# Kernel tuning notes

Hardware: AMD Instinct MI355X
Metric: run time of the kernel (lower is better)

## Reference

```python
import jax, jax.numpy as jnp
import numpy as np

EPS = 1e-05
RMS_EPS = 1e-06


def activation_quant(x, num_bits=8):
    # per-token (last-dim) abs-max int8 fake quant, computed in fp32
    qn = -(2 ** (num_bits - 1))
    qp = 2 ** (num_bits - 1) - 1
    xf = x.astype(jnp.float32)
    s = qp / jnp.clip(jnp.max(jnp.abs(xf), axis=-1, keepdims=True), EPS, None)
    return (jnp.clip(jnp.round(xf * s), qn, qp) / s).astype(x.dtype)


def weight_quant(w):
    # full-tensor abs-mean ternary fake quant
    wf = w.astype(jnp.float32)
    s = 1.0 / jnp.clip(jnp.mean(jnp.abs(wf)), EPS, None)
    return (jnp.clip(jnp.round(wf * s), -1.0, 1.0) / s).astype(w.dtype)


def bit_linear(x, w):
    # STE wrappers (identity in forward value, straight-through in grad)
    qx = x + jax.lax.stop_gradient(activation_quant(x) - x)
    qw = w + jax.lax.stop_gradient(weight_quant(w) - w)
    return jnp.einsum('bsh,oh->bso', qx, qw)


def rms_norm(x, weight, eps=RMS_EPS):
    xf = x.astype(jnp.float32)
    var = jnp.mean(xf * xf, axis=-1, keepdims=True)
    return weight * (xf * jax.lax.rsqrt(var + eps)).astype(x.dtype)


def setup_inputs() -> dict:
    key = jax.random.key(0)
    k1, k2, k3, k4 = jax.random.split(key, 4)
    B, S, H, I = 2, 2048, 2048, 8192
    scale = 1.0 / np.sqrt(H)
    return {
        'x': jax.random.normal(k1, (B, S, H), dtype=jnp.float32),
        'w_gate': jax.random.normal(k2, (I, H), dtype=jnp.float32) * scale,
        'w_up': jax.random.normal(k3, (I, H), dtype=jnp.float32) * scale,
        'w_down': jax.random.normal(k4, (H, I), dtype=jnp.float32) * (1.0 / np.sqrt(I)),
        'ln_weight': jnp.ones((I,), dtype=jnp.float32),
    }


def reference(x, w_gate, w_up, w_down, ln_weight):
    h = jax.nn.silu(bit_linear(x, w_gate)) * bit_linear(x, w_up)
    h = rms_norm(h, ln_weight)
    return bit_linear(h, w_down)
```

## Files before the change

### kernel.cpp

```cpp
#include <hip/hip_runtime.h>
#include <stdint.h>

typedef int v4i __attribute__((ext_vector_type(4)));

#define TOKENS 4096
#define HDIM   2048
#define IDIM   8192
#define WN     16777216
#define NBLK   512
#define BANDP  5e-7f

static __device__ __forceinline__ void gload_lds16(const void* g, void* l) {
  __builtin_amdgcn_global_load_lds(
      (const __attribute__((address_space(1))) void*)(unsigned long long)(uintptr_t)g,
      (__attribute__((address_space(3))) void*)(unsigned)(uintptr_t)l,
      16, 0, 0);
}

static __device__ __forceinline__ double wsum64d(double v) {
#pragma unroll
  for (int m = 32; m; m >>= 1) v += __shfl_xor(v, m, 64);
  return v;
}
static __device__ __forceinline__ double wmax64d(double v) {
#pragma unroll
  for (int m = 32; m; m >>= 1) v = fmax(v, __shfl_xor(v, m, 64));
  return v;
}
static __device__ __forceinline__ float wmax64f(float v) {
#pragma unroll
  for (int m = 32; m; m >>= 1) v = fmaxf(v, __shfl_xor(v, m, 64));
  return v;
}

static __device__ __forceinline__ int q8f(float v, float s, float lo, float hi) {
  float p = v * s;
  return (int)fminf(fmaxf(rintf(p), lo), hi);
}
static __device__ __forceinline__ uint32_t packq_f(float4 v, float s) {
  int a = q8f(v.x, s, -128.f, 127.f);
  int b = q8f(v.y, s, -128.f, 127.f);
  int c = q8f(v.z, s, -128.f, 127.f);
  int d = q8f(v.w, s, -128.f, 127.f);
  return (uint32_t)((a & 255) | ((b & 255) << 8) | ((c & 255) << 16) | ((d & 255) << 24));
}

__global__ __launch_bounds__(256) void wsum_leaf(const float* __restrict__ wg,
                                                 const float* __restrict__ wu,
                                                 const float* __restrict__ wd,
                                                 float* __restrict__ part) {
  const float* w = blockIdx.y == 0 ? wg : (blockIdx.y == 1 ? wu : wd);
  int tid = threadIdx.x;
  const float4* w4 = (const float4*)w;
  size_t base4 = ((size_t)blockIdx.x * 256 + tid) * 32;
  float4 p = w4[base4], q = w4[base4 + 1];
  float r0 = fabsf(p.x), r1 = fabsf(p.y), r2 = fabsf(p.z), r3 = fabsf(p.w);
  float r4 = fabsf(q.x), r5 = fabsf(q.y), r6 = fabsf(q.z), r7 = fabsf(q.w);
  for (int i = 2; i < 32; i += 2) {
    float4 a = w4[base4 + i], b = w4[base4 + i + 1];
    r0 += fabsf(a.x); r1 += fabsf(a.y); r2 += fabsf(a.z); r3 += fabsf(a.w);
    r4 += fabsf(b.x); r5 += fabsf(b.y); r6 += fabsf(b.z); r7 += fabsf(b.w);
  }
  float leaf = ((r0 + r1) + (r2 + r3)) + ((r4 + r5) + (r6 + r7));
  __shared__ float A[256], B[256];
  A[tid] = leaf;
  __syncthreads();
  float* src = A; float* dst = B;
  for (int n = 128; n >= 1; n >>= 1) {
    if (tid < n) dst[tid] = src[2 * tid] + src[2 * tid + 1];
    __syncthreads();
    float* t = src; src = dst; dst = t;
  }
  if (tid == 0) part[blockIdx.y * NBLK + blockIdx.x] = src[0];
}

__global__ __launch_bounds__(256) void wsum_final(const float* __restrict__ part,
                                                  float* __restrict__ wsc) {
  int t = blockIdx.x, tid = threadIdx.x;
  __shared__ float A[512], B[256];
  A[tid] = part[t * NBLK + tid];
  A[tid + 256] = part[t * NBLK + tid + 256];
  __syncthreads();
  float* src = A; float* dst = B;
  for (int n = 256; n >= 1; n >>= 1) {
    if (tid < n) dst[tid] = src[2 * tid] + src[2 * tid + 1];
    __syncthreads();
    float* tmp = src; src = dst; dst = tmp;
  }
  if (tid == 0) {
    float mean32 = src[0] / (float)WN;
    float m32 = fmaxf(mean32, 1e-5f);
    float s32 = 1.0f / m32;
    wsc[t] = s32;
    wsc[3 + t] = 1.0f / s32;
  }
}

__global__ __launch_bounds__(256) void wquant_kernel(const float* __restrict__ wg,
                                                     const float* __restrict__ wu,
                                                     const float* __restrict__ wd,
                                                     const float* __restrict__ wsc,
                                                     int8_t* __restrict__ qg,
                                                     int8_t* __restrict__ qu,
                                                     int8_t* __restrict__ qd) {
  int t = blockIdx.y;
  const float* w = t == 0 ? wg : (t == 1 ? wu : wd);
  int8_t* q = t == 0 ? qg : (t == 1 ? qu : qd);
  float s32 = wsc[t];
  const float4* w4 = (const float4*)w;
  uint32_t* q4 = (uint32_t*)q;
  const int n4 = WN / 4;
  for (int i = blockIdx.x * 256 + threadIdx.x; i < n4; i += gridDim.x * 256) {
    float4 v = w4[i];
    float vv[4] = {v.x, v.y, v.z, v.w};
    int o[4];
#pragma unroll
    for (int j = 0; j < 4; ++j) {
      float pf = fabsf(vv[j]) * s32;
      int q2 = 2 * (int)fminf(rintf(pf), 1.0f);
      if (fabsf(pf - 0.5f) < BANDP) q2 = 1;
      o[j] = (vv[j] < 0.0f) ? -q2 : q2;
    }
    q4[i] = (uint32_t)((o[0] & 255) | ((o[1] & 255) << 8) |
                       ((o[2] & 255) << 16) | ((o[3] & 255) << 24));
  }
}

__global__ __launch_bounds__(256) void xquant_kernel(const float* __restrict__ x,
                                                     int8_t* __restrict__ qx,
                                                     double* __restrict__ axd) {
  int row = blockIdx.x, tid = threadIdx.x;
  const float4* xr = (const float4*)(x + (size_t)row * HDIM);
  float4 v0 = xr[tid], v1 = xr[tid + 256];
  float m = fmaxf(fmaxf(fmaxf(fabsf(v0.x), fabsf(v0.y)), fmaxf(fabsf(v0.z), fabsf(v0.w))),
                  fmaxf(fmaxf(fabsf(v1.x), fabsf(v1.y)), fmaxf(fabsf(v1.z), fabsf(v1.w))));
  m = wmax64f(m);
  __shared__ float red[4];
  int wid = tid >> 6, lane = tid & 63;
  if (lane == 0) red[wid] = m;
  __syncthreads();
  float mm = fmaxf(fmaxf(red[0], red[1]), fmaxf(red[2], red[3]));
  float c32 = fmaxf(mm, 1e-5f);
  float s32 = 127.0f / c32;
  if (tid == 0) axd[row] = 1.0 / (double)s32;
  uint32_t* q4 = (uint32_t*)(qx + (size_t)row * HDIM);
  q4[tid] = packq_f(v0, s32);
  q4[tid + 256] = packq_f(v1, s32);
}

__global__ __launch_bounds__(512, 4) void gemm1_kernel(const int8_t* __restrict__ qx,
                                                       const int8_t* __restrict__ qg,
                                                       const int8_t* __restrict__ qu,
                                                       const float* __restrict__ wsc,
                                                       const double* __restrict__ axd,
                                                       float* __restrict__ h) {
  __shared__ char lds[3 * 8192];
  int tid = threadIdx.x, wid = tid >> 6, lane = tid & 63;
  int l15 = lane & 15, lgp = lane >> 4;
  int wr = wid >> 2, wc = wid & 3;
  int flat = blockIdx.y * 64 + blockIdx.x;
  int nf = (flat & 7) * 256 + (flat >> 3);
  int m0 = (nf >> 6) * 128, n0 = (nf & 63) * 128;
  const int8_t* bA = qx + (size_t)m0 * HDIM;
  const int8_t* bG = qg + (size_t)n0 * HDIM;
  const int8_t* bU = qu + (size_t)n0 * HDIM;

  v4i accg[4][2], accu[4][2];
  v4i vzero = {0, 0, 0, 0};
#pragma unroll
  for (int i = 0; i < 4; ++i)
#pragma unroll
    for (int j = 0; j < 2; ++j) { accg[i][j] = vzero; accu[i][j] = vzero; }

  int aoff[4], goff[2], uoff[2];
#pragma unroll
  for (int i = 0; i < 4; ++i)
    aoff[i] = lgp * 2048 + (wr * 64 + i * 16 + l15) * 16;
#pragma unroll
  for (int i = 0; i < 2; ++i) {
    goff[i] = 8192 + lgp * 2048 + (wc * 32 + i * 16 + l15) * 16;
    uoff[i] = goff[i] + 8192;
  }

  int srow = tid & 127, sslab = tid >> 7;
  char* dA = lds + sslab * 2048 + srow * 16;

  for (int kt = 0; kt < HDIM; kt += 64) {
    __syncthreads();
    size_t koff = (size_t)kt + sslab * 16;
    gload_lds16(bA + (size_t)srow * HDIM + koff, dA);
    gload_lds16(bG + (size_t)srow * HDIM + koff, dA + 8192);
    gload_lds16(bU + (size_t)srow * HDIM + koff, dA + 16384);
    __syncthreads();
    v4i a[4], bg[2], bu[2];
#pragma unroll
    for (int i = 0; i < 4; ++i) a[i] = *(const v4i*)(lds + aoff[i]);
#pragma unroll
    for (int i = 0; i < 2; ++i) {
      bg[i] = *(const v4i*)(lds + goff[i]);
      bu[i] = *(const v4i*)(lds + uoff[i]);
    }
#pragma unroll
    for (int mi = 0; mi < 4; ++mi)
#pragma unroll
      for (int ni = 0; ni < 2; ++ni) {
        accg[mi][ni] = __builtin_amdgcn_mfma_i32_16x16x64_i8(a[mi], bg[ni], accg[mi][ni], 0, 0, 0);
        accu[mi][ni] = __builtin_amdgcn_mfma_i32_16x16x64_i8(a[mi], bu[ni], accu[mi][ni], 0, 0, 0);
      }
  }

  double mg = 0.5 * (double)wsc[3 + 0];
  double mu = 0.5 * (double)wsc[3 + 1];
#pragma unroll
  for (int mi = 0; mi < 4; ++mi) {
#pragma unroll
    for (int rg = 0; rg < 4; ++rg) {
      int grow = m0 + wr * 64 + mi * 16 + lgp * 4 + rg;
      double axr = axd[grow];
      double sg = axr * mg, su = axr * mu;
#pragma unroll
      for (int ni = 0; ni < 2; ++ni) {
        int gcol = n0 + wc * 32 + ni * 16 + l15;
        double g = (double)accg[mi][ni][rg] * sg;
        double u = (double)accu[mi][ni][rg] * su;
        double sig = 1.0 / (1.0 + exp(-g));
        h[(size_t)grow * IDIM + gcol] = (float)((g * sig) * u);
      }
    }
  }
}

__global__ __launch_bounds__(256) void hquant_kernel(const float* __restrict__ h,
                                                     const float* __restrict__ lnw,
                                                     double* __restrict__ ahd,
                                                     int8_t* __restrict__ qh) {
  int row = blockIdx.x, tid = threadIdx.x;
  const float4* hr = (const float4*)(h + (size_t)row * IDIM);
  const float4* lw4 = (const float4*)lnw;
  float4 hv[8], wv[8];
  double ssq = 0.0;
#pragma unroll
  for (int i = 0; i < 8; ++i) {
    hv[i] = hr[tid + i * 256];
    wv[i] = lw4[tid + i * 256];
    ssq += (double)hv[i].x * hv[i].x + (double)hv[i].y * hv[i].y +
           (double)hv[i].z * hv[i].z + (double)hv[i].w * hv[i].w;
  }
  ssq = wsum64d(ssq);
  __shared__ double redd[4];
  __shared__ double redm[4];
  int wid = tid >> 6, lane = tid & 63;
  if (lane == 0) redd[wid] = ssq;
  __syncthreads();
  double tot = redd[0] + redd[1] + redd[2] + redd[3];
  double rd = 1.0 / sqrt(tot * (1.0 / (double)IDIM) + 1e-6);
  double mx = 0.0;
#pragma unroll
  for (int i = 0; i < 8; ++i) {
    double y0 = (double)wv[i].x * ((double)hv[i].x * rd);
    double y1 = (double)wv[i].y * ((double)hv[i].y * rd);
    double y2 = (double)wv[i].z * ((double)hv[i].z * rd);
    double y3 = (double)wv[i].w * ((double)hv[i].w * rd);
    mx = fmax(mx, fmax(fmax(fabs(y0), fabs(y1)), fmax(fabs(y2), fabs(y3))));
  }
  mx = wmax64d(mx);
  if (lane == 0) redm[wid] = mx;
  __syncthreads();
  double mm = fmax(fmax(redm[0], redm[1]), fmax(redm[2], redm[3]));
  float c32 = fmaxf((float)mm, 1e-5f);
  float s32 = 127.0f / c32;
  double sd = (double)s32;
  if (tid == 0) ahd[row] = 1.0 / (double)s32;
  uint32_t* q4 = (uint32_t*)(qh + (size_t)row * IDIM);
#pragma unroll
  for (int i = 0; i < 8; ++i) {
    double y0 = (double)wv[i].x * ((double)hv[i].x * rd);
    double y1 = (double)wv[i].y * ((double)hv[i].y * rd);
    double y2 = (double)wv[i].z * ((double)hv[i].z * rd);
    double y3 = (double)wv[i].w * ((double)hv[i].w * rd);
    int a = (int)fmin(fmax(rint(y0 * sd), -128.0), 127.0);
    int b = (int)fmin(fmax(rint(y1 * sd), -128.0), 127.0);
    int c = (int)fmin(fmax(rint(y2 * sd), -128.0), 127.0);
    int d = (int)fmin(fmax(rint(y3 * sd), -128.0), 127.0);
    q4[tid + i * 256] = (uint32_t)((a & 255) | ((b & 255) << 8) | ((c & 255) << 16) | ((d & 255) << 24));
  }
}

__global__ __launch_bounds__(512, 4) void gemm2_kernel(const int8_t* __restrict__ qh,
                                                       const int8_t* __restrict__ qd,
                                                       const float* __restrict__ wsc,
                                                       const double* __restrict__ ahd,
                                                       float* __restrict__ out) {
  __shared__ char lds[2 * 8192];
  int tid = threadIdx.x, wid = tid >> 6, lane = tid & 63;
  int l15 = lane & 15, lgp = lane >> 4;
  int wr = wid >> 2, wc = wid & 3;
  int flat = blockIdx.y * 16 + blockIdx.x;
  int nf = (flat & 7) * 64 + (flat >> 3);
  int m0 = (nf >> 4) * 128, n0 = (nf & 15) * 128;
  const int8_t* bA = qh + (size_t)m0 * IDIM;
  const int8_t* bB = qd + (size_t)n0 * IDIM;

  v4i acc[4][2];
  v4i vzero = {0, 0, 0, 0};
#pragma unroll
  for (int i = 0; i < 4; ++i)
#pragma unroll
    for (int j = 0; j < 2; ++j) acc[i][j] = vzero;

  int aoff[4], boff[2];
#pragma unroll
  for (int i = 0; i < 4; ++i)
    aoff[i] = lgp * 2048 + (wr * 64 + i * 16 + l15) * 16;
#pragma unroll
  for (int i = 0; i < 2; ++i)
    boff[i] = 8192 + lgp * 2048 + (wc * 32 + i * 16 + l15) * 16;

  int srow = tid & 127, sslab = tid >> 7;
  char* dA = lds + sslab * 2048 + srow * 16;

  for (int kt = 0; kt < IDIM; kt += 64) {
    __syncthreads();
    size_t koff = (size_t)kt + sslab * 16;
    gload_lds16(bA + (size_t)srow * IDIM + koff, dA);
    gload_lds16(bB + (size_t)srow * IDIM + koff, dA + 8192);
    __syncthreads();
    v4i a[4], b[2];
#pragma unroll
    for (int i = 0; i < 4; ++i) a[i] = *(const v4i*)(lds + aoff[i]);
#pragma unroll
    for (int i = 0; i < 2; ++i) b[i] = *(const v4i*)(lds + boff[i]);
#pragma unroll
    for (int mi = 0; mi < 4; ++mi)
#pragma unroll
      for (int ni = 0; ni < 2; ++ni)
        acc[mi][ni] = __builtin_amdgcn_mfma_i32_16x16x64_i8(a[mi], b[ni], acc[mi][ni], 0, 0, 0);
  }

  double md = 0.5 * (double)wsc[3 + 2];
#pragma unroll
  for (int mi = 0; mi < 4; ++mi) {
#pragma unroll
    for (int rg = 0; rg < 4; ++rg) {
      int grow = m0 + wr * 64 + mi * 16 + lgp * 4 + rg;
      double sc = ahd[grow] * md;
#pragma unroll
      for (int ni = 0; ni < 2; ++ni) {
        int gcol = n0 + wc * 32 + ni * 16 + l15;
        out[(size_t)grow * HDIM + gcol] = (float)((double)acc[mi][ni][rg] * sc);
      }
    }
  }
}

extern "C" void kernel_launch(void* const* d_in, const int* in_sizes, int n_in,
                              void* d_out, int out_size, void* d_ws, size_t ws_size,
                              hipStream_t stream) {
  const float* x   = (const float*)d_in[0];
  const float* wg  = (const float*)d_in[1];
  const float* wu  = (const float*)d_in[2];
  const float* wd  = (const float*)d_in[3];
  const float* lnw = (const float*)d_in[4];
  float* out = (float*)d_out;
  char* ws = (char*)d_ws;

  size_t off = 0;
  auto alloc = [&](size_t b) { size_t o = off; off += (b + 255) & ~(size_t)255; return o; };
  size_t o_wsc  = alloc(8 * 4);
  size_t o_part = alloc(3 * NBLK * 4);
  size_t o_axd  = alloc((size_t)TOKENS * 8);
  size_t o_ahd  = alloc((size_t)TOKENS * 8);
  size_t o_qx   = alloc((size_t)TOKENS * HDIM);
  size_t o_qg   = alloc((size_t)IDIM * HDIM);
  size_t o_qu   = alloc((size_t)IDIM * HDIM);
  size_t o_qd   = alloc((size_t)HDIM * IDIM);
  size_t o_h    = alloc((size_t)TOKENS * IDIM * 4);
  (void)ws_size; (void)in_sizes; (void)n_in; (void)out_size; (void)o_qu;

  float* wsc  = (float*)(ws + o_wsc);
  float* part = (float*)(ws + o_part);
  double* axd = (double*)(ws + o_axd);
  double* ahd = (double*)(ws + o_ahd);
  int8_t* qx  = (int8_t*)(ws + o_qx);
  int8_t* qg  = (int8_t*)(ws + o_qg);
  int8_t* qu  = (int8_t*)(ws + o_qu);
  int8_t* qd  = (int8_t*)(ws + o_qd);
  int8_t* qh  = (int8_t*)(ws + o_qg);
  float* h    = (float*)(ws + o_h);

  wsum_leaf<<<dim3(NBLK, 3), 256, 0, stream>>>(wg, wu, wd, part);
  wsum_final<<<3, 256, 0, stream>>>(part, wsc);
  wquant_kernel<<<dim3(1024, 3), 256, 0, stream>>>(wg, wu, wd, wsc, qg, qu, qd);
  xquant_kernel<<<TOKENS, 256, 0, stream>>>(x, qx, axd);
  gemm1_kernel<<<dim3(IDIM / 128, TOKENS / 128), 512, 0, stream>>>(qx, qg, qu, wsc, axd, h);
  hquant_kernel<<<TOKENS, 256, 0, stream>>>(h, lnw, ahd, qh);
  gemm2_kernel<<<dim3(HDIM / 128, TOKENS / 128), 512, 0, stream>>>(qh, qd, wsc, ahd, out);
}
```

Baseline: 543.2 us.

## Double-buffer LDS tiles in both int8 GEMMs to overlap loads with MFMA

Both GEMM kernels now use two LDS buffers: the next K-tile is prefetched via global_load_lds into the alternate buffer while MFMAs consume the current one, cutting one barrier per iteration. Launch bounds are raised from 4 to 6 blocks per CU as an occupancy hint. This doubles LDS per block, which may cap actual occupancy and raise register pressure. Correctness depends on __syncthreads also waiting for the outstanding async LDS loads before the buffer swap.

Result: slower. 1.377 ms (+153.6%).

```diff
diff --git a/kernel.cpp b/kernel.cpp
--- a/kernel.cpp
+++ b/kernel.cpp
@@ -148,13 +148,13 @@
   q4[tid + 256] = packq_f(v1, s32);
 }
 
-__global__ __launch_bounds__(512, 4) void gemm1_kernel(const int8_t* __restrict__ qx,
+__global__ __launch_bounds__(512, 6) void gemm1_kernel(const int8_t* __restrict__ qx,
                                                        const int8_t* __restrict__ qg,
                                                        const int8_t* __restrict__ qu,
                                                        const float* __restrict__ wsc,
                                                        const double* __restrict__ axd,
                                                        float* __restrict__ h) {
-  __shared__ char lds[3 * 8192];
+  __shared__ char lds[2 * 24576];
   int tid = threadIdx.x, wid = tid >> 6, lane = tid & 63;
   int l15 = lane & 15, lgp = lane >> 4;
   int wr = wid >> 2, wc = wid & 3;
@@ -183,22 +183,34 @@
   }
 
   int srow = tid & 127, sslab = tid >> 7;
-  char* dA = lds + sslab * 2048 + srow * 16;
-
-  for (int kt = 0; kt < HDIM; kt += 64) {
-    __syncthreads();
-    size_t koff = (size_t)kt + sslab * 16;
-    gload_lds16(bA + (size_t)srow * HDIM + koff, dA);
-    gload_lds16(bG + (size_t)srow * HDIM + koff, dA + 8192);
-    gload_lds16(bU + (size_t)srow * HDIM + koff, dA + 16384);
-    __syncthreads();
+  char* dA0 = lds + sslab * 2048 + srow * 16;
+  const size_t rA = (size_t)srow * HDIM;
+
+  {
+    size_t koff = (size_t)sslab * 16;
+    gload_lds16(bA + rA + koff, dA0);
+    gload_lds16(bG + rA + koff, dA0 + 8192);
+    gload_lds16(bU + rA + koff, dA0 + 16384);
+  }
+  __syncthreads();
+
+  const int NT = HDIM / 64;
+  int curoff = 0;
+  for (int t = 0; t < NT; ++t) {
+    if (t + 1 < NT) {
+      size_t koff = (size_t)(t + 1) * 64 + sslab * 16;
+      char* d = dA0 + (24576 - curoff);
+      gload_lds16(bA + rA + koff, d);
+      gload_lds16(bG + rA + koff, d + 8192);
+      gload_lds16(bU + rA + koff, d + 16384);
+    }
     v4i a[4], bg[2], bu[2];
 #pragma unroll
-    for (int i = 0; i < 4; ++i) a[i] = *(const v4i*)(lds + aoff[i]);
+    for (int i = 0; i < 4; ++i) a[i] = *(const v4i*)(lds + curoff + aoff[i]);
 #pragma unroll
     for (int i = 0; i < 2; ++i) {
-      bg[i] = *(const v4i*)(lds + goff[i]);
-      bu[i] = *(const v4i*)(lds + uoff[i]);
+      bg[i] = *(const v4i*)(lds + curoff + goff[i]);
+      bu[i] = *(const v4i*)(lds + curoff + uoff[i]);
     }
 #pragma unroll
     for (int mi = 0; mi < 4; ++mi)
@@ -207,6 +219,8 @@
         accg[mi][ni] = __builtin_amdgcn_mfma_i32_16x16x64_i8(a[mi], bg[ni], accg[mi][ni], 0, 0, 0);
         accu[mi][ni] = __builtin_amdgcn_mfma_i32_16x16x64_i8(a[mi], bu[ni], accu[mi][ni], 0, 0, 0);
       }
+    __syncthreads();
+    curoff ^= 24576;
   }
 
   double mg = 0.5 * (double)wsc[3 + 0];
@@ -286,12 +300,12 @@
   }
 }
 
-__global__ __launch_bounds__(512, 4) void gemm2_kernel(const int8_t* __restrict__ qh,
+__global__ __launch_bounds__(512, 6) void gemm2_kernel(const int8_t* __restrict__ qh,
                                                        const int8_t* __restrict__ qd,
                                                        const float* __restrict__ wsc,
                                                        const double* __restrict__ ahd,
                                                        float* __restrict__ out) {
-  __shared__ char lds[2 * 8192];
+  __shared__ char lds[2 * 16384];
   int tid = threadIdx.x, wid = tid >> 6, lane = tid & 63;
   int l15 = lane & 15, lgp = lane >> 4;
   int wr = wid >> 2, wc = wid & 3;
@@ -317,24 +331,37 @@
     boff[i] = 8192 + lgp * 2048 + (wc * 32 + i * 16 + l15) * 16;
 
   int srow = tid & 127, sslab = tid >> 7;
-  char* dA = lds + sslab * 2048 + srow * 16;
-
-  for (int kt = 0; kt < IDIM; kt += 64) {
-    __syncthreads();
-    size_t koff = (size_t)kt + sslab * 16;
-    gload_lds16(bA + (size_t)srow * IDIM + koff, dA);
-    gload_lds16(bB + (size_t)srow * IDIM + koff, dA + 8192);
-    __syncthreads();
+  char* dA0 = lds + sslab * 2048 + srow * 16;
+  const size_t rA = (size_t)srow * IDIM;
+
+  {
+    size_t koff = (size_t)sslab * 16;
+    gload_lds16(bA + rA + koff, dA0);
+    gload_lds16(bB + rA + koff, dA0 + 8192);
+  }
+  __syncthreads();
+
+  const int NT = IDIM / 64;
+  int curoff = 0;
+  for (int t = 0; t < NT; ++t) {
+    if (t + 1 < NT) {
+      size_t koff = (size_t)(t + 1) * 64 + sslab * 16;
+      char* d = dA0 + (16384 - curoff);
+      gload_lds16(bA + rA + koff, d);
+      gload_lds16(bB + rA + koff, d + 8192);
+    }
     v4i a[4], b[2];
 #pragma unroll
-    for (int i = 0; i < 4; ++i) a[i] = *(const v4i*)(lds + aoff[i]);
-#pragma unroll
-    for (int i = 0; i < 2; ++i) b[i] = *(const v4i*)(lds + boff[i]);
+    for (int i = 0; i < 4; ++i) a[i] = *(const v4i*)(lds + curoff + aoff[i]);
+#pragma unroll
+    for (int i = 0; i < 2; ++i) b[i] = *(const v4i*)(lds + curoff + boff[i]);
 #pragma unroll
     for (int mi = 0; mi < 4; ++mi)
 #pragma unroll
       for (int ni = 0; ni < 2; ++ni)
         acc[mi][ni] = __builtin_amdgcn_mfma_i32_16x16x64_i8(a[mi], b[ni], acc[mi][ni], 0, 0, 0);
+    __syncthreads();
+    curoff ^= 16384;
   }
 
   double md = 0.5 * (double)wsc[3 + 2];
```

## Triple-buffer LDS prefetch in both int8 GEMMs and remap tiles per XCD

Applied to the files above, without the earlier changes.

Both GEMM main loops move from load, barrier, compute with a single LDS buffer to a three-stage ring. Tiles two steps ahead are issued via global_load_lds, with explicit vmcnt waits and one barrier per iteration, so global latency overlaps the MFMA work. Block-to-tile mapping is also changed so each XCD gets a contiguous group of N tiles (gemm1) or M tiles (gemm2), aiming for better L2 reuse. LDS use rises to 72KB and 48KB per block, which may cut occupancy below the launch_bounds target of 4 blocks.

Result: faster. 522.8 us (-3.8%).

```diff
diff --git a/kernel.cpp b/kernel.cpp
--- a/kernel.cpp
+++ b/kernel.cpp
@@ -154,13 +154,14 @@
                                                        const float* __restrict__ wsc,
                                                        const double* __restrict__ axd,
                                                        float* __restrict__ h) {
-  __shared__ char lds[3 * 8192];
+  extern __shared__ char lds[];
   int tid = threadIdx.x, wid = tid >> 6, lane = tid & 63;
   int l15 = lane & 15, lgp = lane >> 4;
   int wr = wid >> 2, wc = wid & 3;
   int flat = blockIdx.y * 64 + blockIdx.x;
-  int nf = (flat & 7) * 256 + (flat >> 3);
-  int m0 = (nf >> 6) * 128, n0 = (nf & 63) * 128;
+  int xcd = flat & 7, local = flat >> 3;
+  int mt = local >> 3, nl = local & 7;
+  int m0 = mt * 128, n0 = (xcd * 8 + nl) * 128;
   const int8_t* bA = qx + (size_t)m0 * HDIM;
   const int8_t* bG = qg + (size_t)n0 * HDIM;
   const int8_t* bU = qu + (size_t)n0 * HDIM;
@@ -183,22 +184,39 @@
   }
 
   int srow = tid & 127, sslab = tid >> 7;
-  char* dA = lds + sslab * 2048 + srow * 16;
-
-  for (int kt = 0; kt < HDIM; kt += 64) {
-    __syncthreads();
-    size_t koff = (size_t)kt + sslab * 16;
-    gload_lds16(bA + (size_t)srow * HDIM + koff, dA);
-    gload_lds16(bG + (size_t)srow * HDIM + koff, dA + 8192);
-    gload_lds16(bU + (size_t)srow * HDIM + koff, dA + 16384);
-    __syncthreads();
+  const size_t rA = (size_t)srow * HDIM;
+  int sdst = sslab * 2048 + srow * 16;
+
+  const int NT = HDIM / 64;
+  {
+    size_t k0 = (size_t)sslab * 16;
+    gload_lds16(bA + rA + k0, lds + sdst);
+    gload_lds16(bG + rA + k0, lds + sdst + 8192);
+    gload_lds16(bU + rA + k0, lds + sdst + 16384);
+    size_t k1 = 64 + (size_t)sslab * 16;
+    gload_lds16(bA + rA + k1, lds + 24576 + sdst);
+    gload_lds16(bG + rA + k1, lds + 24576 + sdst + 8192);
+    gload_lds16(bU + rA + k1, lds + 24576 + sdst + 16384);
+  }
+  asm volatile("s_waitcnt vmcnt(3)" ::: "memory");
+  __builtin_amdgcn_s_barrier();
+  __builtin_amdgcn_sched_barrier(0);
+
+  int c0 = 0, c1 = 24576, c2 = 49152;
+  for (int t = 0; t < NT; ++t) {
+    if (t + 2 < NT) {
+      size_t koff = (size_t)(t + 2) * 64 + sslab * 16;
+      gload_lds16(bA + rA + koff, lds + c2 + sdst);
+      gload_lds16(bG + rA + koff, lds + c2 + sdst + 8192);
+      gload_lds16(bU + rA + koff, lds + c2 + sdst + 16384);
+    }
     v4i a[4], bg[2], bu[2];
 #pragma unroll
-    for (int i = 0; i < 4; ++i) a[i] = *(const v4i*)(lds + aoff[i]);
+    for (int i = 0; i < 4; ++i) a[i] = *(const v4i*)(lds + c0 + aoff[i]);
 #pragma unroll
     for (int i = 0; i < 2; ++i) {
-      bg[i] = *(const v4i*)(lds + goff[i]);
-      bu[i] = *(const v4i*)(lds + uoff[i]);
+      bg[i] = *(const v4i*)(lds + c0 + goff[i]);
+      bu[i] = *(const v4i*)(lds + c0 + uoff[i]);
     }
 #pragma unroll
     for (int mi = 0; mi < 4; ++mi)
@@ -207,6 +225,14 @@
         accg[mi][ni] = __builtin_amdgcn_mfma_i32_16x16x64_i8(a[mi], bg[ni], accg[mi][ni], 0, 0, 0);
         accu[mi][ni] = __builtin_amdgcn_mfma_i32_16x16x64_i8(a[mi], bu[ni], accu[mi][ni], 0, 0, 0);
       }
+    __builtin_amdgcn_sched_barrier(0);
+    if (t + 2 < NT)
+      asm volatile("s_waitcnt vmcnt(3)" ::: "memory");
+    else
+      asm volatile("s_waitcnt vmcnt(0)" ::: "memory");
+    __builtin_amdgcn_s_barrier();
+    __builtin_amdgcn_sched_barrier(0);
+    int tmp = c0; c0 = c1; c1 = c2; c2 = tmp;
   }
 
   double mg = 0.5 * (double)wsc[3 + 0];
@@ -291,13 +317,14 @@
                                                        const float* __restrict__ wsc,
                                                        const double* __restrict__ ahd,
                                                        float* __restrict__ out) {
-  __shared__ char lds[2 * 8192];
+  extern __shared__ char lds[];
   int tid = threadIdx.x, wid = tid >> 6, lane = tid & 63;
   int l15 = lane & 15, lgp = lane >> 4;
   int wr = wid >> 2, wc = wid & 3;
   int flat = blockIdx.y * 16 + blockIdx.x;
-  int nf = (flat & 7) * 64 + (flat >> 3);
-  int m0 = (nf >> 4) * 128, n0 = (nf & 15) * 128;
+  int xcd = flat & 7, local = flat >> 3;
+  int mt = xcd * 4 + (local >> 4), nt = local & 15;
+  int m0 = mt * 128, n0 = nt * 128;
   const int8_t* bA = qh + (size_t)m0 * IDIM;
   const int8_t* bB = qd + (size_t)n0 * IDIM;
 
@@ -317,24 +344,47 @@
     boff[i] = 8192 + lgp * 2048 + (wc * 32 + i * 16 + l15) * 16;
 
   int srow = tid & 127, sslab = tid >> 7;
-  char* dA = lds + sslab * 2048 + srow * 16;
-
-  for (int kt = 0; kt < IDIM; kt += 64) {
-    __syncthreads();
-    size_t koff = (size_t)kt + sslab * 16;
-    gload_lds16(bA + (size_t)srow * IDIM + koff, dA);
-    gload_lds16(bB + (size_t)srow * IDIM + koff, dA + 8192);
-    __syncthreads();
+  const size_t rA = (size_t)srow * IDIM;
+  int sdst = sslab * 2048 + srow * 16;
+
+  const int NT = IDIM / 64;
+  {
+    size_t k0 = (size_t)sslab * 16;
+    gload_lds16(bA + rA + k0, lds + sdst);
+    gload_lds16(bB + rA + k0, lds + sdst + 8192);
+    size_t k1 = 64 + (size_t)sslab * 16;
+    gload_lds16(bA + rA + k1, lds + 16384 + sdst);
+    gload_lds16(bB + rA + k1, lds + 16384 + sdst + 8192);
+  }
+  asm volatile("s_waitcnt vmcnt(2)" ::: "memory");
+  __builtin_amdgcn_s_barrier();
+  __builtin_amdgcn_sched_barrier(0);
+
+  int c0 = 0, c1 = 16384, c2 = 32768;
+  for (int t = 0; t < NT; ++t) {
+    if (t + 2 < NT) {
+      size_t koff = (size_t)(t + 2) * 64 + sslab * 16;
+      gload_lds16(bA + rA + koff, lds + c2 + sdst);
+      gload_lds16(bB + rA + koff, lds + c2 + sdst + 8192);
+    }
     v4i a[4], b[2];
 #pragma unroll
-    for (int i = 0; i < 4; ++i) a[i] = *(const v4i*)(lds + aoff[i]);
-#pragma unroll
-    for (int i = 0; i < 2; ++i) b[i] = *(const v4i*)(lds + boff[i]);
+    for (int i = 0; i < 4; ++i) a[i] = *(const v4i*)(lds + c0 + aoff[i]);
+#pragma unroll
+    for (int i = 0; i < 2; ++i) b[i] = *(const v4i*)(lds + c0 + boff[i]);
 #pragma unroll
     for (int mi = 0; mi < 4; ++mi)
 #pragma unroll
       for (int ni = 0; ni < 2; ++ni)
         acc[mi][ni] = __builtin_amdgcn_mfma_i32_16x16x64_i8(a[mi], b[ni], acc[mi][ni], 0, 0, 0);
+    __builtin_amdgcn_sched_barrier(0);
+    if (t + 2 < NT)
+      asm volatile("s_waitcnt vmcnt(2)" ::: "memory");
+    else
+      asm volatile("s_waitcnt vmcnt(0)" ::: "memory");
+    __builtin_amdgcn_s_barrier();
+    __builtin_amdgcn_sched_barrier(0);
+    int tmp = c0; c0 = c1; c1 = c2; c2 = tmp;
   }
 
   double md = 0.5 * (double)wsc[3 + 2];
@@ -392,7 +442,7 @@
   wsum_final<<<3, 256, 0, stream>>>(part, wsc);
   wquant_kernel<<<dim3(1024, 3), 256, 0, stream>>>(wg, wu, wd, wsc, qg, qu, qd);
   xquant_kernel<<<TOKENS, 256, 0, stream>>>(x, qx, axd);
-  gemm1_kernel<<<dim3(IDIM / 128, TOKENS / 128), 512, 0, stream>>>(qx, qg, qu, wsc, axd, h);
+  gemm1_kernel<<<dim3(IDIM / 128, TOKENS / 128), 512, 3 * 24576, stream>>>(qx, qg, qu, wsc, axd, h);
   hquant_kernel<<<TOKENS, 256, 0, stream>>>(h, lnw, ahd, qh);
-  gemm2_kernel<<<dim3(HDIM / 128, TOKENS / 128), 512, 0, stream>>>(qh, qd, wsc, ahd, out);
-}
+  gemm2_kernel<<<dim3(HDIM / 128, TOKENS / 128), 512, 3 * 16384, stream>>>(qh, qd, wsc, ahd, out);
+}
```
